# Performance work log

Hardware: AMD Instinct MI355X
Metric: run time of the kernel (lower is better)

Reference implementation:

```python
import jax, jax.numpy as jnp
import numpy as np

IN_CH = 256
HID = 64
HEADS = 3 * 0 + 4  # num_heads


def setup_inputs() -> dict:
    key = jax.random.key(0)
    ks = jax.random.split(key, 5)
    B, C, H, W = 2, IN_CH, 64, 64
    x = jax.random.normal(ks[0], (B, C, H, W), dtype=jnp.float32)
    # per-head embed conv (kernel 1 -> stored as [heads, 3*HID, C]); kaiming fan_out-ish scale
    w_embed = jax.random.normal(ks[1], (HEADS, 3 * HID, C), dtype=jnp.float32) * np.float32(np.sqrt(2.0 / (3 * HID)))
    b_embed = jnp.zeros((HEADS, 3 * HID), dtype=jnp.float32)
    # output ConvTranspose2d(hidden*heads -> C, kernel 1): weight [hidden*heads, C]
    w_out = jax.random.normal(ks[2], (HEADS * HID, C), dtype=jnp.float32) * np.float32(np.sqrt(2.0 / C))
    b_out = jnp.zeros((C,), dtype=jnp.float32)
    return {"x": x, "w_embed": w_embed, "b_embed": b_embed, "w_out": w_out, "b_out": b_out}


def reference(x, w_embed, b_embed, w_out, b_out):
    B, C, H, W = x.shape
    N = H * W
    nH = w_embed.shape[0]
    D = w_embed.shape[1] // 3
    scale = D ** -0.5
    # 1x1 embed conv per head: [B, nH, 3D, N]
    xf = x.reshape(B, C, N)
    qkv = jnp.einsum('bcn,hdc->bhdn', xf, w_embed) + b_embed[None, :, :, None]
    q, k, v = jnp.split(qkv, 3, axis=2)  # each [B, nH, D, N]
    attn = jnp.einsum('bhci,bhcj->bhij', q, k) * scale  # [B, nH, N, N]
    attn = jax.nn.softmax(attn, axis=-1)
    y = jnp.einsum('bhij,bhcj->bhci', attn, v)  # [B, nH, D, N]
    y = y.reshape(B, nH * D, N)
    # output 1x1 transposed conv (kernel 1 == plain 1x1 projection)
    out = jnp.einsum('bkn,kc->bcn', y, w_out) + b_out[None, :, None]
    out = out.reshape(B, C, H, W)
    return out + x  # residual
```

## Files before the change

kernel.cpp:

```cpp
#include <hip/hip_runtime.h>
#include <hip/hip_bf16.h>

#define NH   4
#define D_   64
#define N_   4096
#define C_   256
#define ME   768

typedef float    f32x4 __attribute__((ext_vector_type(4)));
typedef _Float16 f16x8 __attribute__((ext_vector_type(8)));
typedef _Float16 f16x4 __attribute__((ext_vector_type(4)));

__global__ __launch_bounds__(256) void xt_prep(const float* __restrict__ x,
                                               _Float16* __restrict__ xT) {
    __shared__ float T[64][68];
    const int n0 = blockIdx.x * 64, c0 = blockIdx.y * 64, b = blockIdx.z;
    const int t = threadIdx.x;
    const float* xp = x + ((size_t)b * C_ + c0) * N_ + n0;
    #pragma unroll
    for (int r = 0; r < 4; ++r) {
        int idx = r * 256 + t;
        int c = idx >> 4, ng = (idx & 15) * 4;
        *(f32x4*)&T[c][ng] = *(const f32x4*)(xp + (size_t)c * N_ + ng);
    }
    __syncthreads();
    _Float16* dp = xT + ((size_t)b * N_ + n0) * C_ + c0;
    #pragma unroll
    for (int r = 0; r < 2; ++r) {
        int idx = r * 256 + t;
        int n = idx >> 3, cg = (idx & 7) * 8;
        f16x8 v;
        #pragma unroll
        for (int j = 0; j < 8; ++j) v[j] = (_Float16)T[cg + j][n];
        *(f16x8*)(dp + (size_t)n * C_ + cg) = v;
    }
}

__global__ __launch_bounds__(256) void w_prep(const float* __restrict__ w_embed,
                                              const float* __restrict__ w_out,
                                              _Float16* __restrict__ wh,
                                              _Float16* __restrict__ w_outT) {
    __shared__ float T[64][68];
    const int t = threadIdx.x;
    if (blockIdx.x < 96) {
        int gid = blockIdx.x * 256 + t;
        const float* s = w_embed + (size_t)gid * 8;
        f32x4 a = *(const f32x4*)s, b2 = *(const f32x4*)(s + 4);
        f16x8 v = { (_Float16)a[0], (_Float16)a[1], (_Float16)a[2], (_Float16)a[3],
                    (_Float16)b2[0], (_Float16)b2[1], (_Float16)b2[2], (_Float16)b2[3] };
        *(f16x8*)(wh + (size_t)gid * 8) = v;
    } else {
        int tile = blockIdx.x - 96;
        int tc = tile & 3, tk = tile >> 2;
        #pragma unroll
        for (int r = 0; r < 4; ++r) {
            int idx = r * 256 + t;
            int kl = idx >> 4, cl = (idx & 15) * 4;
            *(f32x4*)&T[kl][cl] = *(const f32x4*)(w_out + (size_t)(tk * 64 + kl) * C_ + tc * 64 + cl);
        }
        __syncthreads();
        #pragma unroll
        for (int r = 0; r < 2; ++r) {
            int idx = r * 256 + t;
            int cl = idx >> 3, kg = (idx & 7) * 8;
            f16x8 v;
            #pragma unroll
            for (int j = 0; j < 8; ++j) v[j] = (_Float16)T[kg + j][cl];
            *(f16x8*)(w_outT + (size_t)(tc * 64 + cl) * C_ + tk * 64 + kg) = v;
        }
    }
}

__global__ __launch_bounds__(256) void qkv_gemm(const _Float16* __restrict__ xT,
                                                const _Float16* __restrict__ wh,
                                                const float* __restrict__ b_embed,
                                                _Float16* __restrict__ qT,
                                                _Float16* __restrict__ kT,
                                                _Float16* __restrict__ vB) {
    __shared__ __align__(16) union SM {
        struct { _Float16 A[64][40], X[64][40]; } s;
        float Os[64][68];
    } sm;
    const int n0 = blockIdx.x * 64, mt = blockIdx.y, b = blockIdx.z;
    const int m0 = mt * 64;
    const int t = threadIdx.x;
    const int lane = t & 63, w = t >> 6, quad = lane >> 4, l16 = lane & 15;
    const int srow = t >> 2, skoff = (t & 3) * 8;
    f32x4 acc[4] = {};
    for (int k0 = 0; k0 < C_; k0 += 32) {
        __syncthreads();
        *(f16x8*)&sm.s.A[srow][skoff] = *(const f16x8*)(wh + (size_t)(m0 + srow) * C_ + k0 + skoff);
        *(f16x8*)&sm.s.X[srow][skoff] = *(const f16x8*)(xT + ((size_t)b * N_ + n0 + srow) * C_ + k0 + skoff);
        __syncthreads();
        f16x8 af = *(const f16x8*)&sm.s.A[w * 16 + l16][quad * 8];
        #pragma unroll
        for (int nb = 0; nb < 4; ++nb) {
            f16x8 bf = *(const f16x8*)&sm.s.X[nb * 16 + l16][quad * 8];
            acc[nb] = __builtin_amdgcn_mfma_f32_16x16x32_f16(af, bf, acc[nb], 0, 0, 0);
        }
    }
    float bias[4];
    #pragma unroll
    for (int rg = 0; rg < 4; ++rg) bias[rg] = b_embed[m0 + w * 16 + quad * 4 + rg];
    __syncthreads();
    #pragma unroll
    for (int nb = 0; nb < 4; ++nb)
        #pragma unroll
        for (int rg = 0; rg < 4; ++rg)
            sm.Os[w * 16 + quad * 4 + rg][nb * 16 + l16] = acc[nb][rg] + bias[rg];
    __syncthreads();
    const int h = mt / 3, r3 = mt - h * 3;
    const int bh = b * NH + h;
    if (r3 < 2) {
        _Float16* dst = (r3 ? kT : qT) + ((size_t)bh * N_ + n0) * D_;
        #pragma unroll
        for (int r = 0; r < 2; ++r) {
            int idx = r * 256 + t;
            int n = idx >> 3, mg = (idx & 7) * 8;
            f16x8 v;
            #pragma unroll
            for (int j = 0; j < 8; ++j) v[j] = (_Float16)sm.Os[mg + j][n];
            *(f16x8*)(dst + (size_t)n * D_ + mg) = v;
        }
    } else {
        _Float16* dst = vB + (size_t)bh * D_ * N_ + n0;
        #pragma unroll
        for (int r = 0; r < 2; ++r) {
            int idx = r * 256 + t;
            int d = idx >> 3, ng = (idx & 7) * 8;
            f32x4 a = *(const f32x4*)&sm.Os[d][ng];
            f32x4 b2 = *(const f32x4*)&sm.Os[d][ng + 4];
            f16x8 v = { (_Float16)a[0], (_Float16)a[1], (_Float16)a[2], (_Float16)a[3],
                        (_Float16)b2[0], (_Float16)b2[1], (_Float16)b2[2], (_Float16)b2[3] };
            *(f16x8*)(dst + (size_t)d * N_ + ng) = v;
        }
    }
}

__global__ __launch_bounds__(256) void attn_kernel(const _Float16* __restrict__ qT,
                                                   const _Float16* __restrict__ kT,
                                                   const _Float16* __restrict__ vB,
                                                   _Float16* __restrict__ opart,
                                                   float* __restrict__ mpart,
                                                   float* __restrict__ lpart) {
    __shared__ __align__(16) union SM {
        struct { _Float16 K[64][72], V[64][72], P[64][72]; } s;
        float Os[64][68];
    } sm;
    const int t = threadIdx.x;
    const int qt = blockIdx.x, h = blockIdx.y;
    const int b = blockIdx.z >> 1, s = blockIdx.z & 1;
    const int bh = b * NH + h, sbh = s * 8 + bh;
    const _Float16* kp = kT + (size_t)bh * N_ * D_;
    const _Float16* vp = vB + (size_t)bh * D_ * N_;
    const int lane = t & 63, w = t >> 6, quad = lane >> 4, l16 = lane & 15;

    const _Float16* qp = qT + ((size_t)bh * N_ + qt * 64 + w * 16 + l16) * D_;
    f16x8 qfrag0 = *(const f16x8*)(qp + quad * 8);
    f16x8 qfrag1 = *(const f16x8*)(qp + 32 + quad * 8);

    f32x4 oacc[4] = {};
    float m_run = -1e30f, l_run = 0.f;

    const int jt0 = s * 32;
    for (int jt = jt0; jt < jt0 + 32; ++jt) {
        __syncthreads();
        #pragma unroll
        for (int r = 0; r < 2; ++r) {
            int idx = r * 256 + t;
            int row = idx >> 3, g = (idx & 7) * 8;
            *(f16x8*)&sm.s.K[row][g] = *(const f16x8*)(kp + (size_t)(jt * 64 + row) * D_ + g);
            *(f16x8*)&sm.s.V[row][g] = *(const f16x8*)(vp + (size_t)row * N_ + jt * 64 + g);
        }
        __syncthreads();

        f32x4 sacc[4] = {};
        #pragma unroll
        for (int jb = 0; jb < 4; ++jb) {
            f16x8 kf0 = *(const f16x8*)&sm.s.K[jb * 16 + l16][quad * 8];
            sacc[jb] = __builtin_amdgcn_mfma_f32_16x16x32_f16(kf0, qfrag0, sacc[jb], 0, 0, 0);
            f16x8 kf1 = *(const f16x8*)&sm.s.K[jb * 16 + l16][32 + quad * 8];
            sacc[jb] = __builtin_amdgcn_mfma_f32_16x16x32_f16(kf1, qfrag1, sacc[jb], 0, 0, 0);
        }

        float mx = fmaxf(fmaxf(sacc[0][0], sacc[0][1]), fmaxf(sacc[0][2], sacc[0][3]));
        #pragma unroll
        for (int jb = 1; jb < 4; ++jb)
            mx = fmaxf(mx, fmaxf(fmaxf(sacc[jb][0], sacc[jb][1]), fmaxf(sacc[jb][2], sacc[jb][3])));
        mx *= 0.125f;
        mx = fmaxf(mx, __shfl_xor(mx, 16));
        mx = fmaxf(mx, __shfl_xor(mx, 32));
        float mnew  = fmaxf(m_run, mx);
        float alpha = __expf(m_run - mnew);
        float p[4][4];
        float rs = 0.f;
        #pragma unroll
        for (int jb = 0; jb < 4; ++jb)
            #pragma unroll
            for (int rg = 0; rg < 4; ++rg) {
                float pv = __expf(sacc[jb][rg] * 0.125f - mnew);
                p[jb][rg] = pv;
                rs += pv;
            }
        rs += __shfl_xor(rs, 16);
        rs += __shfl_xor(rs, 32);
        l_run = l_run * alpha + rs;
        m_run = mnew;

        #pragma unroll
        for (int rg = 0; rg < 4; ++rg) {
            float a4 = __shfl(alpha, quad * 4 + rg);
            #pragma unroll
            for (int db = 0; db < 4; ++db) oacc[db][rg] *= a4;
        }

        #pragma unroll
        for (int jb = 0; jb < 4; ++jb) {
            f16x4 pv = { (_Float16)p[jb][0], (_Float16)p[jb][1],
                         (_Float16)p[jb][2], (_Float16)p[jb][3] };
            *(f16x4*)&sm.s.P[w * 16 + l16][jb * 16 + quad * 4] = pv;
        }

        #pragma unroll
        for (int kc = 0; kc < 2; ++kc) {
            f16x8 pf = *(const f16x8*)&sm.s.P[w * 16 + l16][kc * 32 + quad * 8];
            #pragma unroll
            for (int db = 0; db < 4; ++db) {
                f16x8 vf = *(const f16x8*)&sm.s.V[db * 16 + l16][kc * 32 + quad * 8];
                oacc[db] = __builtin_amdgcn_mfma_f32_16x16x32_f16(pf, vf, oacc[db], 0, 0, 0);
            }
        }
    }

    if (quad == 0) {
        mpart[(size_t)sbh * N_ + qt * 64 + w * 16 + l16] = m_run;
        lpart[(size_t)sbh * N_ + qt * 64 + w * 16 + l16] = l_run;
    }
    __syncthreads();
    #pragma unroll
    for (int db = 0; db < 4; ++db)
        #pragma unroll
        for (int rg = 0; rg < 4; ++rg)
            sm.Os[w * 16 + quad * 4 + rg][db * 16 + l16] = oacc[db][rg];
    __syncthreads();
    _Float16* op = opart + ((size_t)sbh * N_ + qt * 64) * D_;
    #pragma unroll
    for (int r = 0; r < 2; ++r) {
        int idx = r * 256 + t;
        int i = idx >> 3, dg = (idx & 7) * 8;
        f32x4 a = *(const f32x4*)&sm.Os[i][dg];
        f32x4 b2 = *(const f32x4*)&sm.Os[i][dg + 4];
        f16x8 v = { (_Float16)a[0], (_Float16)a[1], (_Float16)a[2], (_Float16)a[3],
                    (_Float16)b2[0], (_Float16)b2[1], (_Float16)b2[2], (_Float16)b2[3] };
        *(f16x8*)(op + (size_t)i * D_ + dg) = v;
    }
}

__global__ __launch_bounds__(256) void combine_kernel(const _Float16* __restrict__ opart,
                                                      const float* __restrict__ mpart,
                                                      const float* __restrict__ lpart,
                                                      _Float16* __restrict__ yT) {
    const int bhi = blockIdx.y;
    const int idx = blockIdx.x * 256 + threadIdx.x;
    const int n = idx >> 3, dg = (idx & 7) * 8;
    const int b = bhi >> 2, h = bhi & 3;
    float m0 = mpart[(size_t)bhi * N_ + n], m1 = mpart[(size_t)(8 + bhi) * N_ + n];
    float l0 = lpart[(size_t)bhi * N_ + n], l1 = lpart[(size_t)(8 + bhi) * N_ + n];
    float M  = fmaxf(m0, m1);
    float w0 = __expf(m0 - M), w1 = __expf(m1 - M);
    float inv = 1.f / (w0 * l0 + w1 * l1);
    w0 *= inv; w1 *= inv;
    f16x8 o0 = *(const f16x8*)(opart + ((size_t)bhi * N_ + n) * D_ + dg);
    f16x8 o1 = *(const f16x8*)(opart + ((size_t)(8 + bhi) * N_ + n) * D_ + dg);
    f16x8 v;
    #pragma unroll
    for (int j = 0; j < 8; ++j)
        v[j] = (_Float16)(w0 * (float)o0[j] + w1 * (float)o1[j]);
    *(f16x8*)(yT + ((size_t)b * N_ + n) * C_ + h * 64 + dg) = v;
}

__global__ __launch_bounds__(256) void proj_gemm(const _Float16* __restrict__ yT,
                                                 const _Float16* __restrict__ w_outT,
                                                 const float* __restrict__ b_out,
                                                 const float* __restrict__ x,
                                                 float* __restrict__ out) {
    __shared__ __align__(16) union SM {
        struct { _Float16 A[64][40], Y[64][40]; } s;
        float Os[64][68];
    } sm;
    const int n0 = blockIdx.x * 64, c0 = blockIdx.y * 64, b = blockIdx.z;
    const int t = threadIdx.x;
    const int lane = t & 63, w = t >> 6, quad = lane >> 4, l16 = lane & 15;
    const int srow = t >> 2, skoff = (t & 3) * 8;
    f32x4 acc[4] = {};
    for (int k0 = 0; k0 < C_; k0 += 32) {
        __syncthreads();
        *(f16x8*)&sm.s.A[srow][skoff] = *(const f16x8*)(w_outT + (size_t)(c0 + srow) * C_ + k0 + skoff);
        *(f16x8*)&sm.s.Y[srow][skoff] = *(const f16x8*)(yT + ((size_t)b * N_ + n0 + srow) * C_ + k0 + skoff);
        __syncthreads();
        f16x8 af = *(const f16x8*)&sm.s.A[w * 16 + l16][quad * 8];
        #pragma unroll
        for (int nb = 0; nb < 4; ++nb) {
            f16x8 bf = *(const f16x8*)&sm.s.Y[nb * 16 + l16][quad * 8];
            acc[nb] = __builtin_amdgcn_mfma_f32_16x16x32_f16(af, bf, acc[nb], 0, 0, 0);
        }
    }
    float bias[4];
    #pragma unroll
    for (int rg = 0; rg < 4; ++rg) bias[rg] = b_out[c0 + w * 16 + quad * 4 + rg];
    __syncthreads();
    #pragma unroll
    for (int nb = 0; nb < 4; ++nb)
        #pragma unroll
        for (int rg = 0; rg < 4; ++rg)
            sm.Os[w * 16 + quad * 4 + rg][nb * 16 + l16] = acc[nb][rg] + bias[rg];
    __syncthreads();
    const float* xp = x + ((size_t)b * C_ + c0) * N_ + n0;
    float* op = out + ((size_t)b * C_ + c0) * N_ + n0;
    #pragma unroll
    for (int r = 0; r < 4; ++r) {
        int idx = r * 256 + t;
        int c = idx >> 4, ng = (idx & 15) * 4;
        f32x4 v  = *(const f32x4*)&sm.Os[c][ng];
        f32x4 xv = *(const f32x4*)(xp + (size_t)c * N_ + ng);
        f32x4 o  = { v[0] + xv[0], v[1] + xv[1], v[2] + xv[2], v[3] + xv[3] };
        *(f32x4*)(op + (size_t)c * N_ + ng) = o;
    }
}

extern "C" void kernel_launch(void* const* d_in, const int* in_sizes, int n_in,
                              void* d_out, int out_size, void* d_ws, size_t ws_size,
                              hipStream_t stream) {
    const float* x       = (const float*)d_in[0];
    const float* w_embed = (const float*)d_in[1];
    const float* b_embed = (const float*)d_in[2];
    const float* w_out   = (const float*)d_in[3];
    const float* b_out   = (const float*)d_in[4];
    float* out = (float*)d_out;

    _Float16* base   = (_Float16*)d_ws;
    _Float16* xT     = base;
    _Float16* wh     = base + 2097152;
    _Float16* w_outT = base + 2293760;
    _Float16* qT     = base + 2359296;
    _Float16* kT     = base + 4456448;
    _Float16* vB     = base + 6553600;
    _Float16* yT     = base + 8650752;
    _Float16* opart  = base + 10747904;
    float*    mpart  = (float*)(base + 14942208);
    float*    lpart  = mpart + 65536;

    xt_prep       <<<dim3(64, 4, 2),  256, 0, stream>>>(x, xT);
    w_prep        <<<dim3(112, 1, 1), 256, 0, stream>>>(w_embed, w_out, wh, w_outT);
    qkv_gemm      <<<dim3(64, 12, 2), 256, 0, stream>>>(xT, wh, b_embed, qT, kT, vB);
    attn_kernel   <<<dim3(64, 4, 4),  256, 0, stream>>>(qT, kT, vB, opart, mpart, lpart);
    combine_kernel<<<dim3(128, 8, 1), 256, 0, stream>>>(opart, mpart, lpart, yT);
    proj_gemm     <<<dim3(64, 4, 2),  256, 0, stream>>>(yT, w_outT, b_out, x, out);
}
```

Before: 169.5 us.

## Rewrite attention with 32x32 MFMA tiles, register P, prefetch, and 3-way KV split

The attention kernel now uses 32x32x16 MFMA instructions, with 128-query tiles per block (32 per wave). The probabilities P are passed to the PV MFMA through lane shuffles in registers instead of a shared-memory round trip, and the scale is folded into Q in the log2 domain so exp2f can be used. The next K/V tile is prefetched into registers while the current one is computed. The KV range is split three ways instead of two, and the combine kernel merges three partials. This aims to cut LDS traffic, softmax ALU work and load latency. The cost is more registers per thread and a larger partial-result workspace.

```diff
diff --git a/kernel.cpp b/kernel.cpp
--- a/kernel.cpp
+++ b/kernel.cpp
@@ -6,10 +6,13 @@
 #define N_   4096
 #define C_   256
 #define ME   768
-
-typedef float    f32x4 __attribute__((ext_vector_type(4)));
-typedef _Float16 f16x8 __attribute__((ext_vector_type(8)));
-typedef _Float16 f16x4 __attribute__((ext_vector_type(4)));
+#define SPLITS 3
+
+typedef float    f32x4  __attribute__((ext_vector_type(4)));
+typedef float    f32x16 __attribute__((ext_vector_type(16)));
+typedef _Float16 f16x8  __attribute__((ext_vector_type(8)));
+typedef _Float16 f16x4  __attribute__((ext_vector_type(4)));
+typedef _Float16 f16x2  __attribute__((ext_vector_type(2)));
 
 __global__ __launch_bounds__(256) void xt_prep(const float* __restrict__ x,
                                                _Float16* __restrict__ xT) {
@@ -144,115 +147,139 @@
                                                    float* __restrict__ mpart,
                                                    float* __restrict__ lpart) {
     __shared__ __align__(16) union SM {
-        struct { _Float16 K[64][72], V[64][72], P[64][72]; } s;
-        float Os[64][68];
+        struct { _Float16 K[64][76], V[64][76]; } s;
+        _Float16 Os[128][76];
     } sm;
     const int t = threadIdx.x;
     const int qt = blockIdx.x, h = blockIdx.y;
-    const int b = blockIdx.z >> 1, s = blockIdx.z & 1;
+    const int b = blockIdx.z / SPLITS, s = blockIdx.z % SPLITS;
     const int bh = b * NH + h, sbh = s * 8 + bh;
     const _Float16* kp = kT + (size_t)bh * N_ * D_;
     const _Float16* vp = vB + (size_t)bh * D_ * N_;
-    const int lane = t & 63, w = t >> 6, quad = lane >> 4, l16 = lane & 15;
-
-    const _Float16* qp = qT + ((size_t)bh * N_ + qt * 64 + w * 16 + l16) * D_;
-    f16x8 qfrag0 = *(const f16x8*)(qp + quad * 8);
-    f16x8 qfrag1 = *(const f16x8*)(qp + 32 + quad * 8);
-
-    f32x4 oacc[4] = {};
-    float m_run = -1e30f, l_run = 0.f;
-
-    const int jt0 = s * 32;
-    for (int jt = jt0; jt < jt0 + 32; ++jt) {
+    const int lane = t & 63, w = t >> 6, l32 = lane & 31, hl = lane >> 5;
+    const bool hl1 = (hl != 0);
+    const int srow = t >> 3, scol = (t & 7) * 8;
+
+    const _Float16* qp = qT + ((size_t)bh * N_ + qt * 128 + w * 32 + l32) * D_;
+    f16x8 qf[4];
+    #pragma unroll
+    for (int kc = 0; kc < 4; ++kc) {
+        qf[kc] = *(const f16x8*)(qp + kc * 16 + hl * 8);
+        qf[kc] *= (_Float16)0.18033688f;
+    }
+
+    f32x16 oacc0 = {}, oacc1 = {};
+    float m_run = -3.0e38f, l_run = 0.f;
+
+    const int jt_lo = (s * 64) / SPLITS, jt_hi = ((s + 1) * 64) / SPLITS;
+    f16x8 kpre[2], vpre[2];
+    #pragma unroll
+    for (int r = 0; r < 2; ++r) {
+        int row = srow + r * 32;
+        kpre[r] = *(const f16x8*)(kp + (size_t)(jt_lo * 64 + row) * D_ + scol);
+        vpre[r] = *(const f16x8*)(vp + (size_t)row * N_ + jt_lo * 64 + scol);
+    }
+
+    for (int jt = jt_lo; jt < jt_hi; ++jt) {
         __syncthreads();
         #pragma unroll
         for (int r = 0; r < 2; ++r) {
-            int idx = r * 256 + t;
-            int row = idx >> 3, g = (idx & 7) * 8;
-            *(f16x8*)&sm.s.K[row][g] = *(const f16x8*)(kp + (size_t)(jt * 64 + row) * D_ + g);
-            *(f16x8*)&sm.s.V[row][g] = *(const f16x8*)(vp + (size_t)row * N_ + jt * 64 + g);
-        }
-        __syncthreads();
-
-        f32x4 sacc[4] = {};
-        #pragma unroll
-        for (int jb = 0; jb < 4; ++jb) {
-            f16x8 kf0 = *(const f16x8*)&sm.s.K[jb * 16 + l16][quad * 8];
-            sacc[jb] = __builtin_amdgcn_mfma_f32_16x16x32_f16(kf0, qfrag0, sacc[jb], 0, 0, 0);
-            f16x8 kf1 = *(const f16x8*)&sm.s.K[jb * 16 + l16][32 + quad * 8];
-            sacc[jb] = __builtin_amdgcn_mfma_f32_16x16x32_f16(kf1, qfrag1, sacc[jb], 0, 0, 0);
-        }
-
-        float mx = fmaxf(fmaxf(sacc[0][0], sacc[0][1]), fmaxf(sacc[0][2], sacc[0][3]));
-        #pragma unroll
-        for (int jb = 1; jb < 4; ++jb)
-            mx = fmaxf(mx, fmaxf(fmaxf(sacc[jb][0], sacc[jb][1]), fmaxf(sacc[jb][2], sacc[jb][3])));
-        mx *= 0.125f;
-        mx = fmaxf(mx, __shfl_xor(mx, 16));
+            int row = srow + r * 32;
+            *(f16x8*)&sm.s.K[row][scol] = kpre[r];
+            *(f16x8*)&sm.s.V[row][scol] = vpre[r];
+        }
+        __syncthreads();
+        if (jt + 1 < jt_hi) {
+            #pragma unroll
+            for (int r = 0; r < 2; ++r) {
+                int row = srow + r * 32;
+                kpre[r] = *(const f16x8*)(kp + (size_t)((jt + 1) * 64 + row) * D_ + scol);
+                vpre[r] = *(const f16x8*)(vp + (size_t)row * N_ + (jt + 1) * 64 + scol);
+            }
+        }
+
+        f32x16 sa0 = {}, sa1 = {};
+        #pragma unroll
+        for (int kc = 0; kc < 4; ++kc) {
+            f16x8 kf0 = *(const f16x8*)&sm.s.K[l32][kc * 16 + hl * 8];
+            sa0 = __builtin_amdgcn_mfma_f32_32x32x16_f16(kf0, qf[kc], sa0, 0, 0, 0);
+            f16x8 kf1 = *(const f16x8*)&sm.s.K[32 + l32][kc * 16 + hl * 8];
+            sa1 = __builtin_amdgcn_mfma_f32_32x32x16_f16(kf1, qf[kc], sa1, 0, 0, 0);
+        }
+
+        float mx = fmaxf(sa0[0], sa0[1]);
+        #pragma unroll
+        for (int r = 2; r < 16; ++r) mx = fmaxf(mx, sa0[r]);
+        #pragma unroll
+        for (int r = 0; r < 16; ++r) mx = fmaxf(mx, sa1[r]);
         mx = fmaxf(mx, __shfl_xor(mx, 32));
         float mnew  = fmaxf(m_run, mx);
-        float alpha = __expf(m_run - mnew);
-        float p[4][4];
+        float alpha = exp2f(m_run - mnew);
         float rs = 0.f;
         #pragma unroll
-        for (int jb = 0; jb < 4; ++jb)
-            #pragma unroll
-            for (int rg = 0; rg < 4; ++rg) {
-                float pv = __expf(sacc[jb][rg] * 0.125f - mnew);
-                p[jb][rg] = pv;
-                rs += pv;
-            }
-        rs += __shfl_xor(rs, 16);
+        for (int r = 0; r < 16; ++r) { sa0[r] = exp2f(sa0[r] - mnew); rs += sa0[r]; }
+        #pragma unroll
+        for (int r = 0; r < 16; ++r) { sa1[r] = exp2f(sa1[r] - mnew); rs += sa1[r]; }
         rs += __shfl_xor(rs, 32);
         l_run = l_run * alpha + rs;
         m_run = mnew;
-
-        #pragma unroll
-        for (int rg = 0; rg < 4; ++rg) {
-            float a4 = __shfl(alpha, quad * 4 + rg);
-            #pragma unroll
-            for (int db = 0; db < 4; ++db) oacc[db][rg] *= a4;
-        }
-
-        #pragma unroll
-        for (int jb = 0; jb < 4; ++jb) {
-            f16x4 pv = { (_Float16)p[jb][0], (_Float16)p[jb][1],
-                         (_Float16)p[jb][2], (_Float16)p[jb][3] };
-            *(f16x4*)&sm.s.P[w * 16 + l16][jb * 16 + quad * 4] = pv;
-        }
-
-        #pragma unroll
-        for (int kc = 0; kc < 2; ++kc) {
-            f16x8 pf = *(const f16x8*)&sm.s.P[w * 16 + l16][kc * 32 + quad * 8];
-            #pragma unroll
-            for (int db = 0; db < 4; ++db) {
-                f16x8 vf = *(const f16x8*)&sm.s.V[db * 16 + l16][kc * 32 + quad * 8];
-                oacc[db] = __builtin_amdgcn_mfma_f32_16x16x32_f16(pf, vf, oacc[db], 0, 0, 0);
+        #pragma unroll
+        for (int r = 0; r < 16; ++r) { oacc0[r] *= alpha; oacc1[r] *= alpha; }
+
+        #pragma unroll
+        for (int jb = 0; jb < 2; ++jb) {
+            const f32x16& sa = jb ? sa1 : sa0;
+            int P[8], X[8];
+            #pragma unroll
+            for (int q = 0; q < 8; ++q) {
+                f16x2 pk = { (_Float16)sa[2 * q], (_Float16)sa[2 * q + 1] };
+                P[q] = __builtin_bit_cast(int, pk);
             }
-        }
-    }
-
-    if (quad == 0) {
-        mpart[(size_t)sbh * N_ + qt * 64 + w * 16 + l16] = m_run;
-        lpart[(size_t)sbh * N_ + qt * 64 + w * 16 + l16] = l_run;
-    }
-    __syncthreads();
-    #pragma unroll
-    for (int db = 0; db < 4; ++db)
-        #pragma unroll
-        for (int rg = 0; rg < 4; ++rg)
-            sm.Os[w * 16 + quad * 4 + rg][db * 16 + l16] = oacc[db][rg];
-    __syncthreads();
-    _Float16* op = opart + ((size_t)sbh * N_ + qt * 64) * D_;
-    #pragma unroll
-    for (int r = 0; r < 2; ++r) {
+            #pragma unroll
+            for (int q = 0; q < 8; ++q) X[q] = __shfl_xor(P[q], 32);
+            union FU { f16x8 v; int d[4]; } f0, f1;
+            f0.d[0] = hl1 ? X[2] : P[0];
+            f0.d[1] = hl1 ? X[3] : P[1];
+            f0.d[2] = hl1 ? P[2] : X[0];
+            f0.d[3] = hl1 ? P[3] : X[1];
+            f1.d[0] = hl1 ? X[6] : P[4];
+            f1.d[1] = hl1 ? X[7] : P[5];
+            f1.d[2] = hl1 ? P[6] : X[4];
+            f1.d[3] = hl1 ? P[7] : X[5];
+            f16x8 vf = *(const f16x8*)&sm.s.V[l32][jb * 32 + hl * 8];
+            oacc0 = __builtin_amdgcn_mfma_f32_32x32x16_f16(vf, f0.v, oacc0, 0, 0, 0);
+            vf = *(const f16x8*)&sm.s.V[l32][jb * 32 + 16 + hl * 8];
+            oacc0 = __builtin_amdgcn_mfma_f32_32x32x16_f16(vf, f1.v, oacc0, 0, 0, 0);
+            vf = *(const f16x8*)&sm.s.V[32 + l32][jb * 32 + hl * 8];
+            oacc1 = __builtin_amdgcn_mfma_f32_32x32x16_f16(vf, f0.v, oacc1, 0, 0, 0);
+            vf = *(const f16x8*)&sm.s.V[32 + l32][jb * 32 + 16 + hl * 8];
+            oacc1 = __builtin_amdgcn_mfma_f32_32x32x16_f16(vf, f1.v, oacc1, 0, 0, 0);
+        }
+    }
+
+    float linv = 1.f / l_run;
+    if (hl == 0) {
+        mpart[(size_t)sbh * N_ + qt * 128 + w * 32 + l32] = m_run;
+        lpart[(size_t)sbh * N_ + qt * 128 + w * 32 + l32] = l_run;
+    }
+    __syncthreads();
+    #pragma unroll
+    for (int db = 0; db < 2; ++db) {
+        const f32x16& oc = db ? oacc1 : oacc0;
+        #pragma unroll
+        for (int rq = 0; rq < 4; ++rq) {
+            f16x4 pv = { (_Float16)(oc[rq * 4 + 0] * linv), (_Float16)(oc[rq * 4 + 1] * linv),
+                         (_Float16)(oc[rq * 4 + 2] * linv), (_Float16)(oc[rq * 4 + 3] * linv) };
+            *(f16x4*)&sm.Os[w * 32 + l32][db * 32 + rq * 8 + hl * 4] = pv;
+        }
+    }
+    __syncthreads();
+    _Float16* op = opart + ((size_t)sbh * N_ + qt * 128) * D_;
+    #pragma unroll
+    for (int r = 0; r < 4; ++r) {
         int idx = r * 256 + t;
-        int i = idx >> 3, dg = (idx & 7) * 8;
-        f32x4 a = *(const f32x4*)&sm.Os[i][dg];
-        f32x4 b2 = *(const f32x4*)&sm.Os[i][dg + 4];
-        f16x8 v = { (_Float16)a[0], (_Float16)a[1], (_Float16)a[2], (_Float16)a[3],
-                    (_Float16)b2[0], (_Float16)b2[1], (_Float16)b2[2], (_Float16)b2[3] };
-        *(f16x8*)(op + (size_t)i * D_ + dg) = v;
+        int i = idx >> 3, ch = (idx & 7) * 8;
+        *(f16x8*)(op + (size_t)i * D_ + ch) = *(const f16x8*)&sm.Os[i][ch];
     }
 }
 
@@ -264,18 +291,23 @@
     const int idx = blockIdx.x * 256 + threadIdx.x;
     const int n = idx >> 3, dg = (idx & 7) * 8;
     const int b = bhi >> 2, h = bhi & 3;
-    float m0 = mpart[(size_t)bhi * N_ + n], m1 = mpart[(size_t)(8 + bhi) * N_ + n];
-    float l0 = lpart[(size_t)bhi * N_ + n], l1 = lpart[(size_t)(8 + bhi) * N_ + n];
-    float M  = fmaxf(m0, m1);
-    float w0 = __expf(m0 - M), w1 = __expf(m1 - M);
-    float inv = 1.f / (w0 * l0 + w1 * l1);
-    w0 *= inv; w1 *= inv;
+    float m0 = mpart[(size_t)bhi * N_ + n];
+    float m1 = mpart[(size_t)(8 + bhi) * N_ + n];
+    float m2 = mpart[(size_t)(16 + bhi) * N_ + n];
+    float l0 = lpart[(size_t)bhi * N_ + n];
+    float l1 = lpart[(size_t)(8 + bhi) * N_ + n];
+    float l2 = lpart[(size_t)(16 + bhi) * N_ + n];
+    float M  = fmaxf(m0, fmaxf(m1, m2));
+    float w0 = exp2f(m0 - M) * l0, w1 = exp2f(m1 - M) * l1, w2 = exp2f(m2 - M) * l2;
+    float inv = 1.f / (w0 + w1 + w2);
+    w0 *= inv; w1 *= inv; w2 *= inv;
     f16x8 o0 = *(const f16x8*)(opart + ((size_t)bhi * N_ + n) * D_ + dg);
     f16x8 o1 = *(const f16x8*)(opart + ((size_t)(8 + bhi) * N_ + n) * D_ + dg);
+    f16x8 o2 = *(const f16x8*)(opart + ((size_t)(16 + bhi) * N_ + n) * D_ + dg);
     f16x8 v;
     #pragma unroll
     for (int j = 0; j < 8; ++j)
-        v[j] = (_Float16)(w0 * (float)o0[j] + w1 * (float)o1[j]);
+        v[j] = (_Float16)(w0 * (float)o0[j] + w1 * (float)o1[j] + w2 * (float)o2[j]);
     *(f16x8*)(yT + ((size_t)b * N_ + n) * C_ + h * 64 + dg) = v;
 }
 
@@ -347,13 +379,13 @@
     _Float16* vB     = base + 6553600;
     _Float16* yT     = base + 8650752;
     _Float16* opart  = base + 10747904;
-    float*    mpart  = (float*)(base + 14942208);
-    float*    lpart  = mpart + 65536;
+    float*    mpart  = (float*)(base + 17039360);
+    float*    lpart  = mpart + 98304;
 
     xt_prep       <<<dim3(64, 4, 2),  256, 0, stream>>>(x, xT);
     w_prep        <<<dim3(112, 1, 1), 256, 0, stream>>>(w_embed, w_out, wh, w_outT);
     qkv_gemm      <<<dim3(64, 12, 2), 256, 0, stream>>>(xT, wh, b_embed, qT, kT, vB);
-    attn_kernel   <<<dim3(64, 4, 4),  256, 0, stream>>>(qT, kT, vB, opart, mpart, lpart);
+    attn_kernel   <<<dim3(32, 4, 6),  256, 0, stream>>>(qT, kT, vB, opart, mpart, lpart);
     combine_kernel<<<dim3(128, 8, 1), 256, 0, stream>>>(opart, mpart, lpart, yT);
     proj_gemm     <<<dim3(64, 4, 2),  256, 0, stream>>>(yT, w_outT, b_out, x, out);
 }
```

Result: no change. 169.1 us (-0.2%).
